# Performance work log

Measured on AMD Instinct MI355X. Metric: run time of the kernel, lower is better.

Reference implementation:

```python
import jax, jax.numpy as jnp
import numpy as np

PATCH = 5
CHANNELS = 1

def _conv_valid(x, w):
    # x: [B,C,H,W], w: [O,I,kh,kw], VALID padding, stride 1
    return jax.lax.conv_general_dilated(
        x, w, window_strides=(1, 1), padding='VALID',
        dimension_numbers=('NCHW', 'OIHW', 'NCHW'))

def setup_inputs() -> dict:
    key = jax.random.key(0)
    kx, ky = jax.random.split(key)
    B, C, H, W = 16, CHANNELS, 1024, 1024
    x = jax.random.normal(kx, (B, C, H, W), dtype=jnp.float32)
    y = jax.random.normal(ky, (B, C, H, W), dtype=jnp.float32)
    # box-mean kernel: all ones / p^2
    mean_mask = jnp.full((C, C, PATCH, PATCH), 1.0 / (PATCH * PATCH), dtype=jnp.float32)
    # center-pixel extraction kernel
    ones_mask = jnp.zeros((C, C, PATCH, PATCH), dtype=jnp.float32).at[:, :, PATCH // 2, PATCH // 2].set(1.0)
    return {"x": x, "y": y, "mean_mask": mean_mask, "ones_mask": ones_mask}

def reference(x, y, mean_mask, ones_mask):
    # (center(x) - boxmean(x)) * (center(y) - boxmean(y)), then box-mean -> local covariance
    xc = _conv_valid(x, ones_mask) - _conv_valid(x, mean_mask)   # [B,C,H-4,W-4]
    yc = _conv_valid(y, ones_mask) - _conv_valid(y, mean_mask)
    return _conv_valid(xc * yc, mean_mask)                        # [B,C,H-8,W-8]
```

## Files before the change

### kernel.cpp

```cpp
#include <hip/hip_runtime.h>


#define W 1024
#define H 1024
#define OW 1016
#define OH 1016
#define NBATCH 16
#define NSTRIP 5
#define NCHUNK 64
#define RCHUNK 16
#define NSTEP (RCHUNK + 8)
#define STRIP_OUT 248

typedef float floatx4 __attribute__((ext_vector_type(4)));

__device__ __forceinline__ float shfl_up1(float v) { return __shfl_up(v, 1, 64); }
__device__ __forceinline__ float shfl_dn1(float v) { return __shfl_down(v, 1, 64); }

__global__ __launch_bounds__(256, 4) void cov_kernel(
    const float* __restrict__ x, const float* __restrict__ y,
    float* __restrict__ out)
{
    const int wid  = (blockIdx.x << 2) + (threadIdx.x >> 6);
    const int lane = threadIdx.x & 63;

    const int chunk = wid & (NCHUNK - 1);
    const int rest  = wid >> 6;
    const int strip = rest % NSTRIP;
    const int batch = rest / NSTRIP;

    const int o0   = chunk * RCHUNK;
    const int base = strip * STRIP_OUT;

    int col4 = base + (lane << 2);
    if (col4 > W - 4) col4 = W - 4;

    const float* __restrict__ xb = x + (size_t)batch * H * W;
    const float* __restrict__ yb = y + (size_t)batch * H * W;
    float* __restrict__ ob = out + (size_t)batch * OH * OW;

    const int j4 = base + ((lane - 1) << 2);
    const bool lane_ok = (lane >= 1) && (lane <= 62) && (j4 <= OW - 4);

    constexpr float inv25 = 1.0f / 25.0f;

    float4 xr[5], yr[5], pr[5];
    float4 vx = make_float4(0.f, 0.f, 0.f, 0.f);
    float4 vy = vx, vp = vx;
    #pragma unroll
    for (int u = 0; u < 5; ++u) { xr[u] = vx; yr[u] = vx; pr[u] = vx; }

    float4 xn_n, yn_n;
    {
        int r = o0; if (r > H - 1) r = H - 1;
        const int off = r * W + col4;
        xn_n = *(const float4*)(xb + off);
        yn_n = *(const float4*)(yb + off);
    }

    #pragma unroll
    for (int s = 0; s < NSTEP; ++s) {
        const int u = s % 5;
        const float4 xn = xn_n;
        const float4 yn = yn_n;

        if (s + 1 < NSTEP) {
            int rn = o0 + s + 1; if (rn > H - 1) rn = H - 1;
            const int offn = rn * W + col4;
            xn_n = *(const float4*)(xb + offn);
            yn_n = *(const float4*)(yb + offn);
        }

        vx.x += xn.x - xr[u].x; vx.y += xn.y - xr[u].y;
        vx.z += xn.z - xr[u].z; vx.w += xn.w - xr[u].w;
        vy.x += yn.x - yr[u].x; vy.y += yn.y - yr[u].y;
        vy.z += yn.z - yr[u].z; vy.w += yn.w - yr[u].w;
        xr[u] = xn; yr[u] = yn;

        const float vxl0 = shfl_up1(vx.z), vxl1 = shfl_up1(vx.w);
        const float vxr0 = shfl_dn1(vx.x), vxr1 = shfl_dn1(vx.y);
        const float vyl0 = shfl_up1(vy.z), vyl1 = shfl_up1(vy.w);
        const float vyr0 = shfl_dn1(vy.x), vyr1 = shfl_dn1(vy.y);

        const float hx0 = vxl0 + vxl1 + vx.x + vx.y + vx.z;
        const float hx1 = hx0 - vxl0 + vx.w;
        const float hx2 = hx1 - vxl1 + vxr0;
        const float hx3 = hx2 - vx.x + vxr1;
        const float hy0 = vyl0 + vyl1 + vy.x + vy.y + vy.z;
        const float hy1 = hy0 - vyl0 + vy.w;
        const float hy2 = hy1 - vyl1 + vyr0;
        const float hy3 = hy2 - vy.x + vyr1;

        const float4 cx4 = xr[(u + 3) % 5];
        const float4 cy4 = yr[(u + 3) % 5];

        float4 p;
        p.x = (cx4.x - hx0 * inv25) * (cy4.x - hy0 * inv25);
        p.y = (cx4.y - hx1 * inv25) * (cy4.y - hy1 * inv25);
        p.z = (cx4.z - hx2 * inv25) * (cy4.z - hy2 * inv25);
        p.w = (cx4.w - hx3 * inv25) * (cy4.w - hy3 * inv25);

        vp.x += p.x - pr[u].x; vp.y += p.y - pr[u].y;
        vp.z += p.z - pr[u].z; vp.w += p.w - pr[u].w;
        pr[u] = p;

        const int i = o0 + s - 8;
        if (s >= 8 && i < OH) {
            const float vpl0 = shfl_up1(vp.z), vpl1 = shfl_up1(vp.w);
            const float vpr0 = shfl_dn1(vp.x), vpr1 = shfl_dn1(vp.y);
            const float h0 = vpl0 + vpl1 + vp.x + vp.y + vp.z;
            const float h1 = h0 - vpl0 + vp.w;
            const float h2 = h1 - vpl1 + vpr0;
            const float h3 = h2 - vp.x + vpr1;
            if (lane_ok) {
                floatx4 o4 = { h0 * inv25, h1 * inv25, h2 * inv25, h3 * inv25 };
                __builtin_nontemporal_store(o4, (floatx4*)(ob + (size_t)i * OW + j4));
            }
        }
    }
}

extern "C" void kernel_launch(void* const* d_in, const int* in_sizes, int n_in,
                              void* d_out, int out_size, void* d_ws, size_t ws_size,
                              hipStream_t stream) {
    const float* x = (const float*)d_in[0];
    const float* y = (const float*)d_in[1];
    float* out = (float*)d_out;

    dim3 grid(NBATCH * NSTRIP * NCHUNK / 4);
    dim3 block(256);
    hipLaunchKernelGGL(cov_kernel, grid, block, 0, stream, x, y, out);
}
```

Baseline: 203.1 us.

## Replace register ring buffers with global reloads and LDS product ring, stop unrolling

The x/y five-row register rings are removed. The outgoing row is reloaded from global memory (likely an L2/cache hit), and the center row is kept in a two-deep register shift. The product ring moves to LDS, the step loop is no longer unrolled, and the min-blocks launch bound is dropped. The aim is lower register pressure, smaller code and higher occupancy, at the cost of twice as many global loads, LDS traffic and loop overhead.

```diff
diff --git a/kernel.cpp b/kernel.cpp
--- a/kernel.cpp
+++ b/kernel.cpp
@@ -17,12 +17,15 @@
 __device__ __forceinline__ float shfl_up1(float v) { return __shfl_up(v, 1, 64); }
 __device__ __forceinline__ float shfl_dn1(float v) { return __shfl_down(v, 1, 64); }
 
-__global__ __launch_bounds__(256, 4) void cov_kernel(
+__global__ __launch_bounds__(256) void cov_kernel(
     const float* __restrict__ x, const float* __restrict__ y,
     float* __restrict__ out)
 {
+    __shared__ float4 pring[4 * 5 * 64];
+
     const int wid  = (blockIdx.x << 2) + (threadIdx.x >> 6);
     const int lane = threadIdx.x & 63;
+    const int wib  = threadIdx.x >> 6;
 
     const int chunk = wid & (NCHUNK - 1);
     const int rest  = wid >> 6;
@@ -44,13 +47,14 @@
 
     constexpr float inv25 = 1.0f / 25.0f;
 
-    float4 xr[5], yr[5], pr[5];
-    float4 vx = make_float4(0.f, 0.f, 0.f, 0.f);
-    float4 vy = vx, vp = vx;
-    #pragma unroll
-    for (int u = 0; u < 5; ++u) { xr[u] = vx; yr[u] = vx; pr[u] = vx; }
+    float4 z4 = make_float4(0.f, 0.f, 0.f, 0.f);
+    float4 vx = z4, vy = z4, vp = z4;
+    float4 cxA = z4, cxB = z4, cyA = z4, cyB = z4;
 
-    float4 xn_n, yn_n;
+    float4* const prw = &pring[wib * 5 * 64 + lane];
+    int u5 = 0;
+
+    float4 xn_n, yn_n, xo_n = z4, yo_n = z4;
     {
         int r = o0; if (r > H - 1) r = H - 1;
         const int off = r * W + col4;
@@ -58,63 +62,81 @@
         yn_n = *(const float4*)(yb + off);
     }
 
-    #pragma unroll
+    #pragma unroll 1
     for (int s = 0; s < NSTEP; ++s) {
-        const int u = s % 5;
-        const float4 xn = xn_n;
-        const float4 yn = yn_n;
+        const float4 xn = xn_n, yn = yn_n;
+        const float4 xo = xo_n, yo = yo_n;
 
         if (s + 1 < NSTEP) {
             int rn = o0 + s + 1; if (rn > H - 1) rn = H - 1;
             const int offn = rn * W + col4;
             xn_n = *(const float4*)(xb + offn);
             yn_n = *(const float4*)(yb + offn);
+            if (s + 1 >= 5) {
+                int ro = o0 + s - 4; if (ro > H - 1) ro = H - 1;
+                const int offo = ro * W + col4;
+                xo_n = *(const float4*)(xb + offo);
+                yo_n = *(const float4*)(yb + offo);
+            }
         }
 
-        vx.x += xn.x - xr[u].x; vx.y += xn.y - xr[u].y;
-        vx.z += xn.z - xr[u].z; vx.w += xn.w - xr[u].w;
-        vy.x += yn.x - yr[u].x; vy.y += yn.y - yr[u].y;
-        vy.z += yn.z - yr[u].z; vy.w += yn.w - yr[u].w;
-        xr[u] = xn; yr[u] = yn;
+        if (s >= 5) {
+            vx.x += xn.x - xo.x; vx.y += xn.y - xo.y;
+            vx.z += xn.z - xo.z; vx.w += xn.w - xo.w;
+            vy.x += yn.x - yo.x; vy.y += yn.y - yo.y;
+            vy.z += yn.z - yo.z; vy.w += yn.w - yo.w;
+        } else {
+            vx.x += xn.x; vx.y += xn.y; vx.z += xn.z; vx.w += xn.w;
+            vy.x += yn.x; vy.y += yn.y; vy.z += yn.z; vy.w += yn.w;
+        }
 
-        const float vxl0 = shfl_up1(vx.z), vxl1 = shfl_up1(vx.w);
-        const float vxr0 = shfl_dn1(vx.x), vxr1 = shfl_dn1(vx.y);
-        const float vyl0 = shfl_up1(vy.z), vyl1 = shfl_up1(vy.w);
-        const float vyr0 = shfl_dn1(vy.x), vyr1 = shfl_dn1(vy.y);
+        const float4 cx4 = cxB, cy4 = cyB;
+        cxB = cxA; cyB = cyA; cxA = xn; cyA = yn;
 
-        const float hx0 = vxl0 + vxl1 + vx.x + vx.y + vx.z;
-        const float hx1 = hx0 - vxl0 + vx.w;
-        const float hx2 = hx1 - vxl1 + vxr0;
-        const float hx3 = hx2 - vx.x + vxr1;
-        const float hy0 = vyl0 + vyl1 + vy.x + vy.y + vy.z;
-        const float hy1 = hy0 - vyl0 + vy.w;
-        const float hy2 = hy1 - vyl1 + vyr0;
-        const float hy3 = hy2 - vy.x + vyr1;
+        if (s >= 4) {
+            const float vxl0 = shfl_up1(vx.z), vxl1 = shfl_up1(vx.w);
+            const float vxr0 = shfl_dn1(vx.x), vxr1 = shfl_dn1(vx.y);
+            const float vyl0 = shfl_up1(vy.z), vyl1 = shfl_up1(vy.w);
+            const float vyr0 = shfl_dn1(vy.x), vyr1 = shfl_dn1(vy.y);
 
-        const float4 cx4 = xr[(u + 3) % 5];
-        const float4 cy4 = yr[(u + 3) % 5];
+            const float hx0 = vxl0 + vxl1 + vx.x + vx.y + vx.z;
+            const float hx1 = hx0 - vxl0 + vx.w;
+            const float hx2 = hx1 - vxl1 + vxr0;
+            const float hx3 = hx2 - vx.x + vxr1;
+            const float hy0 = vyl0 + vyl1 + vy.x + vy.y + vy.z;
+            const float hy1 = hy0 - vyl0 + vy.w;
+            const float hy2 = hy1 - vyl1 + vyr0;
+            const float hy3 = hy2 - vy.x + vyr1;
 
-        float4 p;
-        p.x = (cx4.x - hx0 * inv25) * (cy4.x - hy0 * inv25);
-        p.y = (cx4.y - hx1 * inv25) * (cy4.y - hy1 * inv25);
-        p.z = (cx4.z - hx2 * inv25) * (cy4.z - hy2 * inv25);
-        p.w = (cx4.w - hx3 * inv25) * (cy4.w - hy3 * inv25);
+            float4 p;
+            p.x = (cx4.x - hx0 * inv25) * (cy4.x - hy0 * inv25);
+            p.y = (cx4.y - hx1 * inv25) * (cy4.y - hy1 * inv25);
+            p.z = (cx4.z - hx2 * inv25) * (cy4.z - hy2 * inv25);
+            p.w = (cx4.w - hx3 * inv25) * (cy4.w - hy3 * inv25);
 
-        vp.x += p.x - pr[u].x; vp.y += p.y - pr[u].y;
-        vp.z += p.z - pr[u].z; vp.w += p.w - pr[u].w;
-        pr[u] = p;
+            float4* const pslot = prw + u5 * 64;
+            if (s >= 9) {
+                const float4 pold = *pslot;
+                vp.x += p.x - pold.x; vp.y += p.y - pold.y;
+                vp.z += p.z - pold.z; vp.w += p.w - pold.w;
+            } else {
+                vp.x += p.x; vp.y += p.y; vp.z += p.z; vp.w += p.w;
+            }
+            *pslot = p;
+            if (++u5 == 5) u5 = 0;
 
-        const int i = o0 + s - 8;
-        if (s >= 8 && i < OH) {
-            const float vpl0 = shfl_up1(vp.z), vpl1 = shfl_up1(vp.w);
-            const float vpr0 = shfl_dn1(vp.x), vpr1 = shfl_dn1(vp.y);
-            const float h0 = vpl0 + vpl1 + vp.x + vp.y + vp.z;
-            const float h1 = h0 - vpl0 + vp.w;
-            const float h2 = h1 - vpl1 + vpr0;
-            const float h3 = h2 - vp.x + vpr1;
-            if (lane_ok) {
-                floatx4 o4 = { h0 * inv25, h1 * inv25, h2 * inv25, h3 * inv25 };
-                __builtin_nontemporal_store(o4, (floatx4*)(ob + (size_t)i * OW + j4));
+            const int i = o0 + s - 8;
+            if (s >= 8 && i < OH) {
+                const float vpl0 = shfl_up1(vp.z), vpl1 = shfl_up1(vp.w);
+                const float vpr0 = shfl_dn1(vp.x), vpr1 = shfl_dn1(vp.y);
+                const float h0 = vpl0 + vpl1 + vp.x + vp.y + vp.z;
+                const float h1 = h0 - vpl0 + vp.w;
+                const float h2 = h1 - vpl1 + vpr0;
+                const float h3 = h2 - vp.x + vpr1;
+                if (lane_ok) {
+                    floatx4 o4 = { h0 * inv25, h1 * inv25, h2 * inv25, h3 * inv25 };
+                    __builtin_nontemporal_store(o4, (floatx4*)(ob + (size_t)i * OW + j4));
+                }
             }
         }
     }
```

Measured after the change: 195.9 us. -3.5%, faster.

## Move p ring buffer to LDS and reload old rows instead of register rings

Applied to the files above, without the earlier changes.

Replaces the per-thread register rings for x, y and the product with a ring held in shared memory for the product. The row leaving the window is re-read from global memory (expected to hit in cache) rather than kept in registers. The warm-up steps are specialised so they skip the shuffles and subtractions that have no effect, the centre/mean math uses FMAs, and the min-occupancy launch bound is dropped. The aim is to cut register pressure and wasted warm-up work, at the cost of extra global loads and LDS traffic.

```diff
diff --git a/kernel.cpp b/kernel.cpp
--- a/kernel.cpp
+++ b/kernel.cpp
@@ -17,12 +17,15 @@
 __device__ __forceinline__ float shfl_up1(float v) { return __shfl_up(v, 1, 64); }
 __device__ __forceinline__ float shfl_dn1(float v) { return __shfl_down(v, 1, 64); }
 
-__global__ __launch_bounds__(256, 4) void cov_kernel(
+__global__ __launch_bounds__(256) void cov_kernel(
     const float* __restrict__ x, const float* __restrict__ y,
     float* __restrict__ out)
 {
+    __shared__ float4 pring[4 * 5 * 64];
+
     const int wid  = (blockIdx.x << 2) + (threadIdx.x >> 6);
     const int lane = threadIdx.x & 63;
+    const int wib  = threadIdx.x >> 6;
 
     const int chunk = wid & (NCHUNK - 1);
     const int rest  = wid >> 6;
@@ -44,13 +47,13 @@
 
     constexpr float inv25 = 1.0f / 25.0f;
 
-    float4 xr[5], yr[5], pr[5];
-    float4 vx = make_float4(0.f, 0.f, 0.f, 0.f);
-    float4 vy = vx, vp = vx;
-    #pragma unroll
-    for (int u = 0; u < 5; ++u) { xr[u] = vx; yr[u] = vx; pr[u] = vx; }
+    const float4 z4 = make_float4(0.f, 0.f, 0.f, 0.f);
+    float4 vx = z4, vy = z4, vp = z4;
+    float4 cxA = z4, cxB = z4, cyA = z4, cyB = z4;
 
-    float4 xn_n, yn_n;
+    float4* const prw = &pring[wib * 5 * 64 + lane];
+
+    float4 xn_n, yn_n, xo_n = z4, yo_n = z4;
     {
         int r = o0; if (r > H - 1) r = H - 1;
         const int off = r * W + col4;
@@ -58,66 +61,92 @@
         yn_n = *(const float4*)(yb + off);
     }
 
+#define STEPX(SRT, COLDPF, CSUB, CP, CRD, SLOT, CEMIT) do {                    \
+    const float4 xn = xn_n, yn = yn_n;                                         \
+    const float4 xo = xo_n, yo = yo_n;                                         \
+    { int rn_ = o0 + (SRT) + 1; if (rn_ > H - 1) rn_ = H - 1;                  \
+      const size_t ro4_ = (size_t)rn_ * W + col4;                              \
+      xn_n = *(const float4*)(xb + ro4_);                                      \
+      yn_n = *(const float4*)(yb + ro4_); }                                    \
+    if (COLDPF) {                                                              \
+      int ro_ = o0 + (SRT) - 4; if (ro_ > H - 1) ro_ = H - 1;                  \
+      const size_t rr4_ = (size_t)ro_ * W + col4;                              \
+      xo_n = *(const float4*)(xb + rr4_);                                      \
+      yo_n = *(const float4*)(yb + rr4_); }                                    \
+    if (CSUB) {                                                                \
+      vx.x += xn.x - xo.x; vx.y += xn.y - xo.y;                                \
+      vx.z += xn.z - xo.z; vx.w += xn.w - xo.w;                                \
+      vy.x += yn.x - yo.x; vy.y += yn.y - yo.y;                                \
+      vy.z += yn.z - yo.z; vy.w += yn.w - yo.w;                                \
+    } else {                                                                   \
+      vx.x += xn.x; vx.y += xn.y; vx.z += xn.z; vx.w += xn.w;                  \
+      vy.x += yn.x; vy.y += yn.y; vy.z += yn.z; vy.w += yn.w;                  \
+    }                                                                          \
+    const float4 cx4 = cxB, cy4 = cyB;                                         \
+    cxB = cxA; cyB = cyA; cxA = xn; cyA = yn;                                  \
+    if (CP) {                                                                  \
+      const float vxl0 = shfl_up1(vx.z), vxl1 = shfl_up1(vx.w);                \
+      const float vyl0 = shfl_up1(vy.z), vyl1 = shfl_up1(vy.w);                \
+      const float vxr0 = shfl_dn1(vx.x), vxr1 = shfl_dn1(vx.y);                \
+      const float vyr0 = shfl_dn1(vy.x), vyr1 = shfl_dn1(vy.y);                \
+      const float hx0 = vxl0 + vxl1 + vx.x + vx.y + vx.z;                      \
+      const float hx1 = hx0 - vxl0 + vx.w;                                     \
+      const float hx2 = hx1 - vxl1 + vxr0;                                     \
+      const float hx3 = hx2 - vx.x + vxr1;                                     \
+      const float hy0 = vyl0 + vyl1 + vy.x + vy.y + vy.z;                      \
+      const float hy1 = hy0 - vyl0 + vy.w;                                     \
+      const float hy2 = hy1 - vyl1 + vyr0;                                     \
+      const float hy3 = hy2 - vy.x + vyr1;                                     \
+      float4 p;                                                                \
+      p.x = __builtin_fmaf(-inv25, hx0, cx4.x) * __builtin_fmaf(-inv25, hy0, cy4.x); \
+      p.y = __builtin_fmaf(-inv25, hx1, cx4.y) * __builtin_fmaf(-inv25, hy1, cy4.y); \
+      p.z = __builtin_fmaf(-inv25, hx2, cx4.z) * __builtin_fmaf(-inv25, hy2, cy4.z); \
+      p.w = __builtin_fmaf(-inv25, hx3, cx4.w) * __builtin_fmaf(-inv25, hy3, cy4.w); \
+      float4* const pslot_ = prw + (SLOT) * 64;                                \
+      if (CRD) {                                                               \
+        const float4 pold_ = *pslot_;          \
+        vp.x += p.x - pold_.x; vp.y += p.y - pold_.y;                          \
+        vp.z += p.z - pold_.z; vp.w += p.w - pold_.w;                          \
+      } else {                                                                 \
+        vp.x += p.x; vp.y += p.y; vp.z += p.z; vp.w += p.w;                    \
+      }                                                                        \
+      *pslot_ = p;                                          \
+      if (CEMIT) {                                                             \
+        const int i_ = o0 + (SRT) - 8;                                         \
+        const float vpl0 = shfl_up1(vp.z), vpl1 = shfl_up1(vp.w);              \
+        const float vpr0 = shfl_dn1(vp.x), vpr1 = shfl_dn1(vp.y);              \
+        const float h0 = vpl0 + vpl1 + vp.x + vp.y + vp.z;                     \
+        const float h1 = h0 - vpl0 + vp.w;                                     \
+        const float h2 = h1 - vpl1 + vpr0;                                     \
+        const float h3 = h2 - vp.x + vpr1;                                     \
+        if (lane_ok && i_ < OH) {                                              \
+          floatx4 o4_ = { h0 * inv25, h1 * inv25, h2 * inv25, h3 * inv25 };    \
+          __builtin_nontemporal_store(o4_, (floatx4*)(ob + (size_t)i_ * OW + j4)); \
+        }                                                                      \
+      }                                                                        \
+    }                                                                          \
+} while (0)
+
+    STEPX(0, false, false, false, false, 0, false);
+    STEPX(1, false, false, false, false, 0, false);
+    STEPX(2, false, false, false, false, 0, false);
+    STEPX(3, false, false, false, false, 0, false);
+    STEPX(4, true,  false, true,  false, 0, false);
+    STEPX(5, true,  true,  true,  false, 1, false);
+    STEPX(6, true,  true,  true,  false, 2, false);
+    STEPX(7, true,  true,  true,  false, 3, false);
+    STEPX(8, true,  true,  true,  false, 4, true);
+
     #pragma unroll
-    for (int s = 0; s < NSTEP; ++s) {
-        const int u = s % 5;
-        const float4 xn = xn_n;
-        const float4 yn = yn_n;
-
-        if (s + 1 < NSTEP) {
-            int rn = o0 + s + 1; if (rn > H - 1) rn = H - 1;
-            const int offn = rn * W + col4;
-            xn_n = *(const float4*)(xb + offn);
-            yn_n = *(const float4*)(yb + offn);
-        }
-
-        vx.x += xn.x - xr[u].x; vx.y += xn.y - xr[u].y;
-        vx.z += xn.z - xr[u].z; vx.w += xn.w - xr[u].w;
-        vy.x += yn.x - yr[u].x; vy.y += yn.y - yr[u].y;
-        vy.z += yn.z - yr[u].z; vy.w += yn.w - yr[u].w;
-        xr[u] = xn; yr[u] = yn;
-
-        const float vxl0 = shfl_up1(vx.z), vxl1 = shfl_up1(vx.w);
-        const float vxr0 = shfl_dn1(vx.x), vxr1 = shfl_dn1(vx.y);
-        const float vyl0 = shfl_up1(vy.z), vyl1 = shfl_up1(vy.w);
-        const float vyr0 = shfl_dn1(vy.x), vyr1 = shfl_dn1(vy.y);
-
-        const float hx0 = vxl0 + vxl1 + vx.x + vx.y + vx.z;
-        const float hx1 = hx0 - vxl0 + vx.w;
-        const float hx2 = hx1 - vxl1 + vxr0;
-        const float hx3 = hx2 - vx.x + vxr1;
-        const float hy0 = vyl0 + vyl1 + vy.x + vy.y + vy.z;
-        const float hy1 = hy0 - vyl0 + vy.w;
-        const float hy2 = hy1 - vyl1 + vyr0;
-        const float hy3 = hy2 - vy.x + vyr1;
-
-        const float4 cx4 = xr[(u + 3) % 5];
-        const float4 cy4 = yr[(u + 3) % 5];
-
-        float4 p;
-        p.x = (cx4.x - hx0 * inv25) * (cy4.x - hy0 * inv25);
-        p.y = (cx4.y - hx1 * inv25) * (cy4.y - hy1 * inv25);
-        p.z = (cx4.z - hx2 * inv25) * (cy4.z - hy2 * inv25);
-        p.w = (cx4.w - hx3 * inv25) * (cy4.w - hy3 * inv25);
-
-        vp.x += p.x - pr[u].x; vp.y += p.y - pr[u].y;
-        vp.z += p.z - pr[u].z; vp.w += p.w - pr[u].w;
-        pr[u] = p;
-
-        const int i = o0 + s - 8;
-        if (s >= 8 && i < OH) {
-            const float vpl0 = shfl_up1(vp.z), vpl1 = shfl_up1(vp.w);
-            const float vpr0 = shfl_dn1(vp.x), vpr1 = shfl_dn1(vp.y);
-            const float h0 = vpl0 + vpl1 + vp.x + vp.y + vp.z;
-            const float h1 = h0 - vpl0 + vp.w;
-            const float h2 = h1 - vpl1 + vpr0;
-            const float h3 = h2 - vp.x + vpr1;
-            if (lane_ok) {
-                floatx4 o4 = { h0 * inv25, h1 * inv25, h2 * inv25, h3 * inv25 };
-                __builtin_nontemporal_store(o4, (floatx4*)(ob + (size_t)i * OW + j4));
-            }
-        }
+    for (int k = 0; k < 3; ++k) {
+        const int sb = 9 + 5 * k;
+        STEPX(sb + 0, true, true, true, true, 0, true);
+        STEPX(sb + 1, true, true, true, true, 1, true);
+        STEPX(sb + 2, true, true, true, true, 2, true);
+        STEPX(sb + 3, true, true, true, true, 3, true);
+        STEPX(sb + 4, true, true, true, true, 4, true);
     }
+#undef STEPX
 }
 
 extern "C" void kernel_launch(void* const* d_in, const int* in_sizes, int n_in,
```

New measurement: 191.1 us. 5.9% less time.
